# Optimization experiments

Measured on AMD Instinct MI355X. Metric: run time of the kernel, lower is better.

Reference implementation:

```python
import jax, jax.numpy as jnp
import numpy as np

B, N, D, H = 32, 64, 128, 256
LN_EPS = 1e-5


def _mlp(x, W1, b1, g, beta, W2, b2):
    # Linear -> LayerNorm -> GELU (exact erf) -> Linear
    h = x @ W1 + b1
    mu = jnp.mean(h, axis=-1, keepdims=True)
    var = jnp.var(h, axis=-1, keepdims=True)
    h = (h - mu) * jax.lax.rsqrt(var + LN_EPS) * g + beta
    h = jax.nn.gelu(h, approximate=False)
    return h @ W2 + b2


def setup_inputs() -> dict:
    key = jax.random.key(0)
    ks = jax.random.split(key, 10)
    s = lambda fan_in: 1.0 / np.sqrt(fan_in)
    return {
        "slots": jax.random.normal(ks[0], (B, N, D), dtype=jnp.float32),
        "adjacency": jax.random.uniform(ks[1], (B, N, N), dtype=jnp.float32),
        # edge_net params
        "We1": jax.random.uniform(ks[2], (2 * D, H), minval=-s(2 * D), maxval=s(2 * D), dtype=jnp.float32),
        "be1": jnp.zeros((H,), jnp.float32),
        "ge": jnp.ones((H,), jnp.float32),
        "bge": jnp.zeros((H,), jnp.float32),
        "We2": jax.random.uniform(ks[3], (H, D), minval=-s(H), maxval=s(H), dtype=jnp.float32),
        "be2": jnp.zeros((D,), jnp.float32),
        # node_net params
        "Wn1": jax.random.uniform(ks[4], (2 * D, H), minval=-s(2 * D), maxval=s(2 * D), dtype=jnp.float32),
        "bn1": jnp.zeros((H,), jnp.float32),
        "gn": jnp.ones((H,), jnp.float32),
        "bgn": jnp.zeros((H,), jnp.float32),
        "Wn2": jax.random.uniform(ks[5], (H, D), minval=-s(H), maxval=s(H), dtype=jnp.float32),
        "bn2": jnp.zeros((D,), jnp.float32),
    }


def reference(slots, adjacency, We1, be1, ge, bge, We2, be2, Wn1, bn1, gn, bgn, Wn2, bn2):
    b, n, d = slots.shape
    # all-pairs edge features: receiver i, sender j -> [B,N,N,2D]
    ei = jnp.broadcast_to(slots[:, :, None, :], (b, n, n, d))
    ej = jnp.broadcast_to(slots[:, None, :, :], (b, n, n, d))
    edge_feat = jnp.concatenate([ei, ej], axis=-1)
    edge_out = _mlp(edge_feat, We1, be1, ge, bge, We2, be2)  # [B,N,N,D]
    # mask diagonal (i != j) and weight by adjacency, then reduce over j
    mask = 1.0 - jnp.eye(n, dtype=slots.dtype)
    w = adjacency * mask  # [B,N,N]
    messages = jnp.einsum('bij,bijd->bid', w, edge_out)
    node_input = jnp.concatenate([slots, messages], axis=-1)
    delta = _mlp(node_input, Wn1, bn1, gn, bgn, Wn2, bn2)
    return slots + delta
```

## Files before the change

### kernel.cpp

```cpp
#include <hip/hip_runtime.h>

#define NB 32
#define NN 64
#define ND 128
#define NH 256
#define LN_EPS 1e-5f
#define RP 4

__device__ __forceinline__ float gelu2(float x) {
    const float au = fabsf(x);
    const float z  = au * 0.70710678118654752440f;
    float p = fmaf(0.078108f, z, 0.000972f);
    p = fmaf(p, z, 0.230389f);
    p = fmaf(p, z, 0.278393f);
    p = fmaf(p, z, 1.0f);
    const float p2 = p * p;
    const float r  = __builtin_amdgcn_rcpf(p2 * p2);
    return (x + au) - au * r;
}
__device__ __forceinline__ float gelu_h(float x) { return 0.5f * gelu2(x); }

__global__ __launch_bounds__(256) void k_pre(const float* __restrict__ slots,
                                             const float* __restrict__ We1,
                                             const float* __restrict__ be1,
                                             const float* __restrict__ Wn1,
                                             const float* __restrict__ We2,
                                             const float* __restrict__ be2,
                                             float* __restrict__ Pt,
                                             float* __restrict__ Qm,
                                             float* __restrict__ XW,
                                             float4* __restrict__ rowstats,
                                             float* __restrict__ WC,
                                             float* __restrict__ v) {
    __shared__ float xs[RP][ND];
    __shared__ float red[4][RP][4];
    const int t = threadIdx.x;

    if (blockIdx.x >= 512) {
        const int bid2 = blockIdx.x - 512;
        if (bid2 == 64) {
            __shared__ float bs[ND];
            if (t < ND) bs[t] = be2[t];
            __syncthreads();
            float acc = 0.f;
            #pragma unroll 4
            for (int d = 0; d < ND; ++d) acc = fmaf(bs[d], Wn1[(ND + d) * NH + t], acc);
            v[t] = acc;
            return;
        }
        const int k0 = bid2 * 4;
        __shared__ float ws[4][ND];
        #pragma unroll
        for (int i = 0; i < 2; ++i) {
            const int idx = t + i * 256;
            ws[idx >> 7][idx & 127] = We2[(k0 + (idx >> 7)) * ND + (idx & 127)];
        }
        __syncthreads();
        float acc[4] = {0.f, 0.f, 0.f, 0.f};
        #pragma unroll 4
        for (int d = 0; d < ND; ++d) {
            const float wn = Wn1[(ND + d) * NH + t];
            #pragma unroll
            for (int r = 0; r < 4; ++r) acc[r] = fmaf(ws[r][d], wn, acc[r]);
        }
        #pragma unroll
        for (int r = 0; r < 4; ++r) WC[(k0 + r) * NH + t] = acc[r];
        return;
    }

    const int r0 = blockIdx.x * RP;
    const int lane = t & 63, wave = t >> 6;
    #pragma unroll
    for (int i = 0; i < 2; ++i) {
        const int idx = t + i * 256;
        xs[idx >> 7][idx & 127] = slots[(size_t)(r0 + (idx >> 7)) * ND + (idx & 127)];
    }
    __syncthreads();
    float pt[RP], qq[RP], xw[RP];
    const float bb = be1[t];
    #pragma unroll
    for (int r = 0; r < RP; ++r) { pt[r] = bb; qq[r] = 0.f; xw[r] = 0.f; }
    #pragma unroll 4
    for (int d = 0; d < ND; ++d) {
        const float wt  = We1[d * NH + t];
        const float wbt = We1[(ND + d) * NH + t];
        const float wn  = Wn1[d * NH + t];
        #pragma unroll
        for (int r = 0; r < RP; ++r) {
            const float x = xs[r][d];
            pt[r] = fmaf(x, wt,  pt[r]);
            qq[r] = fmaf(x, wbt, qq[r]);
            xw[r] = fmaf(x, wn,  xw[r]);
        }
    }
    #pragma unroll
    for (int r = 0; r < RP; ++r) {
        const size_t row = (size_t)(r0 + r);
        Pt[row * NH + t] = pt[r];
        Qm[row * NH + t] = qq[r];
        XW[row * NH + t] = xw[r];
    }
    float s1[RP], s2[RP], s3[RP], s4[RP];
    #pragma unroll
    for (int r = 0; r < RP; ++r) {
        s1[r] = pt[r]; s2[r] = pt[r] * pt[r];
        s3[r] = qq[r]; s4[r] = qq[r] * qq[r];
    }
    #pragma unroll
    for (int off = 32; off; off >>= 1) {
        #pragma unroll
        for (int r = 0; r < RP; ++r) {
            s1[r] += __shfl_xor(s1[r], off);
            s2[r] += __shfl_xor(s2[r], off);
            s3[r] += __shfl_xor(s3[r], off);
            s4[r] += __shfl_xor(s4[r], off);
        }
    }
    if (lane == 0) {
        #pragma unroll
        for (int r = 0; r < RP; ++r) {
            red[wave][r][0] = s1[r]; red[wave][r][1] = s2[r];
            red[wave][r][2] = s3[r]; red[wave][r][3] = s4[r];
        }
    }
    __syncthreads();
    if (t < RP) {
        float4 st;
        st.x = (red[0][t][0] + red[1][t][0]) + (red[2][t][0] + red[3][t][0]);
        st.y = (red[0][t][1] + red[1][t][1]) + (red[2][t][1] + red[3][t][1]);
        st.z = (red[0][t][2] + red[1][t][2]) + (red[2][t][2] + red[3][t][2]);
        st.w = (red[0][t][3] + red[1][t][3]) + (red[2][t][3] + red[3][t][3]);
        rowstats[r0 + t] = st;
    }
}

__global__ __launch_bounds__(256) void k_msg(
    const float* __restrict__ adj,
    const float* __restrict__ Pt,
    const float* __restrict__ Qm,
    const float4* __restrict__ rowstats,
    const float* __restrict__ ge,  const float* __restrict__ bge,
    float* __restrict__ Sw, float* __restrict__ wsumw)
{
    __shared__ float  lds_pt[NH];
    __shared__ float4 lds_wmr[NN];
    __shared__ float  lds_s[4][NH];

    const int row = blockIdx.x;
    const int b   = row >> 6;
    const int i   = row & 63;
    const int t   = threadIdx.x;
    const int lane = t & 63;
    const int wave = t >> 6;

    lds_pt[t] = Pt[(size_t)row * NH + t];
    __syncthreads();

    const int jp = t >> 2, part = t & 3;
    {
        float cd = 0.f;
        const float4* qrow = (const float4*)(Qm + ((size_t)b * NN + jp) * NH) + part * 16;
        const float4* pr   = (const float4*)lds_pt + part * 16;
        #pragma unroll 4
        for (int k = 0; k < 16; ++k) {
            const float4 q = qrow[k];
            const float4 p = pr[k];
            cd = fmaf(p.x, q.x, fmaf(p.y, q.y, fmaf(p.z, q.z, fmaf(p.w, q.w, cd))));
        }
        cd += __shfl_xor(cd, 1); cd += __shfl_xor(cd, 2);
        if (part == 0) {
            const float inv = 1.0f / NH;
            const float4 stj = rowstats[(size_t)b * NN + jp];
            const float4 sti = rowstats[row];
            float a = adj[(size_t)row * NN + jp];
            if (jp == i) a = 0.f;
            const float mu = (sti.x + stj.z) * inv;
            const float e2 = fmaf(2.f, cd, sti.y + stj.w) * inv;
            const float rr = __builtin_amdgcn_rsqf(fmaf(-mu, mu, e2) + LN_EPS);
            lds_wmr[jp] = make_float4(0.5f * a, rr, -mu * rr, a);
        }
    }
    __syncthreads();

    if (wave == 0) {
        float wv = lds_wmr[lane].w;
        #pragma unroll
        for (int off = 32; off; off >>= 1) wv += __shfl_xor(wv, off);
        if (lane == 0) wsumw[row] = wv;
    }

    const float4 P  = ((const float4*)lds_pt)[lane];
    const float4 G  = ((const float4*)ge)[lane];
    const float4 Bg = ((const float4*)bge)[lane];
    const float4* Qb = (const float4*)(Qm + (size_t)b * NN * NH);
    float4 A = make_float4(0.f, 0.f, 0.f, 0.f);
    #pragma unroll 4
    for (int jj = wave; jj < NN; jj += 4) {
        const float4 q = Qb[jj * (NH / 4) + lane];
        const float4 m = lds_wmr[jj];
        float h, u0, u;
        h = P.x + q.x; u0 = fmaf(h, m.y, m.z); u = fmaf(u0, G.x, Bg.x); A.x = fmaf(m.x, gelu2(u), A.x);
        h = P.y + q.y; u0 = fmaf(h, m.y, m.z); u = fmaf(u0, G.y, Bg.y); A.y = fmaf(m.x, gelu2(u), A.y);
        h = P.z + q.z; u0 = fmaf(h, m.y, m.z); u = fmaf(u0, G.z, Bg.z); A.z = fmaf(m.x, gelu2(u), A.z);
        h = P.w + q.w; u0 = fmaf(h, m.y, m.z); u = fmaf(u0, G.w, Bg.w); A.w = fmaf(m.x, gelu2(u), A.w);
    }
    ((float4*)lds_s[wave])[lane] = A;
    __syncthreads();
    Sw[(size_t)row * NH + t] =
        (lds_s[0][t] + lds_s[1][t]) + (lds_s[2][t] + lds_s[3][t]);
}

__global__ __launch_bounds__(512) void k_node(
    const float* __restrict__ slots,
    const float* __restrict__ Sw, const float* __restrict__ wsumw,
    const float* __restrict__ XW,
    const float* __restrict__ WC, const float* __restrict__ v,
    const float* __restrict__ bn1,
    const float* __restrict__ gn,  const float* __restrict__ bgn,
    const float* __restrict__ Wn2, const float* __restrict__ bn2,
    float* __restrict__ out)
{
    __shared__ float lds_S[4][NH];
    __shared__ float lds_part[4][NH];
    __shared__ float lds_g[4][NH];
    __shared__ float lds_red[4][4][2];
    __shared__ float lds_mr[4][2];

    const int r0   = blockIdx.x * 4;
    const int t    = threadIdx.x;
    const int c    = t & 255;
    const int kh   = t >> 8;
    const int lane = t & 63;
    const int wave = t >> 6;

    lds_S[kh * 2 + 0][c] = Sw[(size_t)(r0 + kh * 2 + 0) * NH + c];
    lds_S[kh * 2 + 1][c] = Sw[(size_t)(r0 + kh * 2 + 1) * NH + c];
    __syncthreads();

    float acc[4] = {0.f, 0.f, 0.f, 0.f};
    {
        const float* wc = WC + (size_t)kh * 128 * NH + c;
        #pragma unroll 8
        for (int k = 0; k < 128; ++k) {
            const float w = wc[k * NH];
            const int kk = kh * 128 + k;
            acc[0] = fmaf(lds_S[0][kk], w, acc[0]);
            acc[1] = fmaf(lds_S[1][kk], w, acc[1]);
            acc[2] = fmaf(lds_S[2][kk], w, acc[2]);
            acc[3] = fmaf(lds_S[3][kk], w, acc[3]);
        }
    }
    if (kh == 1) {
        #pragma unroll
        for (int r = 0; r < 4; ++r) lds_part[r][c] = acc[r];
    }
    __syncthreads();

    float h[4];
    if (kh == 0) {
        const float b1 = bn1[c], vc = v[c];
        #pragma unroll
        for (int r = 0; r < 4; ++r)
            h[r] = acc[r] + lds_part[r][c] + fmaf(wsumw[r0 + r], vc, b1)
                 + XW[(size_t)(r0 + r) * NH + c];
        float s1[4], s2[4];
        #pragma unroll
        for (int r = 0; r < 4; ++r) { s1[r] = h[r]; s2[r] = h[r] * h[r]; }
        #pragma unroll
        for (int off = 32; off; off >>= 1) {
            #pragma unroll
            for (int r = 0; r < 4; ++r) {
                s1[r] += __shfl_xor(s1[r], off);
                s2[r] += __shfl_xor(s2[r], off);
            }
        }
        if (lane == 0) {
            #pragma unroll
            for (int r = 0; r < 4; ++r) { lds_red[wave][r][0] = s1[r]; lds_red[wave][r][1] = s2[r]; }
        }
    }
    __syncthreads();
    if (t < 4) {
        const float S1 = (lds_red[0][t][0] + lds_red[1][t][0]) + (lds_red[2][t][0] + lds_red[3][t][0]);
        const float S2 = (lds_red[0][t][1] + lds_red[1][t][1]) + (lds_red[2][t][1] + lds_red[3][t][1]);
        const float mu  = S1 * (1.0f / NH);
        const float var = fmaf(-mu, mu, S2 * (1.0f / NH));
        lds_mr[t][0] = mu;
        lds_mr[t][1] = __builtin_amdgcn_rsqf(var + LN_EPS);
    }
    __syncthreads();
    if (kh == 0) {
        const float g = gn[c], bg = bgn[c];
        #pragma unroll
        for (int r = 0; r < 4; ++r) {
            const float rr = lds_mr[r][1];
            const float u0 = fmaf(h[r], rr, -lds_mr[r][0] * rr);
            lds_g[r][c] = gelu_h(fmaf(u0, g, bg));
        }
    }
    __syncthreads();

    {
        const int rg = t >> 7, c2 = t & 127;
        float da = 0.f, db = 0.f;
        const float* w2 = Wn2 + c2;
        const float* gr = lds_g[rg];
        #pragma unroll 8
        for (int k = 0; k < NH; k += 2) {
            da = fmaf(gr[k],     w2[k * ND],       da);
            db = fmaf(gr[k + 1], w2[(k + 1) * ND], db);
        }
        const size_t o = (size_t)(r0 + rg) * ND + c2;
        out[o] = slots[o] + bn2[c2] + da + db;
    }
}

extern "C" void kernel_launch(void* const* d_in, const int* in_sizes, int n_in,
                              void* d_out, int out_size, void* d_ws, size_t ws_size,
                              hipStream_t stream) {
    const float* slots = (const float*)d_in[0];
    const float* adj   = (const float*)d_in[1];
    const float* We1   = (const float*)d_in[2];
    const float* be1   = (const float*)d_in[3];
    const float* ge    = (const float*)d_in[4];
    const float* bge   = (const float*)d_in[5];
    const float* We2   = (const float*)d_in[6];
    const float* be2   = (const float*)d_in[7];
    const float* Wn1   = (const float*)d_in[8];
    const float* bn1   = (const float*)d_in[9];
    const float* gn    = (const float*)d_in[10];
    const float* bgn   = (const float*)d_in[11];
    const float* Wn2   = (const float*)d_in[12];
    const float* bn2   = (const float*)d_in[13];
    float* out = (float*)d_out;

    const size_t RN = (size_t)NB * NN;
    float*  Ptw   = (float*)d_ws;
    float*  Qw    = Ptw   + RN * NH;
    float*  XWw   = Qw    + RN * NH;
    float*  Sww   = XWw   + RN * NH;
    float*  wsumw = Sww   + RN * NH;
    float*  WCw   = wsumw + RN;
    float*  vw    = WCw   + (size_t)NH * NH;
    float4* rsw   = (float4*)(vw + NH);

    k_pre <<<577,          256, 0, stream>>>(slots, We1, be1, Wn1, We2, be2,
                                             Ptw, Qw, XWw, rsw, WCw, vw);
    k_msg <<<(int)RN,      256, 0, stream>>>(adj, Ptw, Qw, rsw, ge, bge, Sww, wsumw);
    k_node<<<(int)(RN / 4), 512, 0, stream>>>(slots, Sww, wsumw, XWw, WCw, vw,
                                              bn1, gn, bgn, Wn2, bn2, out);
}
```

Measured before the change: 62.72 us.

## Estrin GELU polynomial, occupancy hint, unroll tweaks, split-K float4 Wn2 GEMV

The GELU erf polynomial is re-evaluated in Estrin form to shorten the dependency chain. k_msg gets a min-blocks-per-CU launch bound and a fixed-trip loop with a pre-offset pointer. Unroll factors grow in k_pre and k_node. The final Wn2 product in k_node is split four ways over K with float4 weight loads, then reduced through shared memory. This costs an extra barrier and LDS buffer and may raise register pressure.

New measurement: 68.09 us. +8.6%, slower.

```diff
diff --git a/kernel.cpp b/kernel.cpp
--- a/kernel.cpp
+++ b/kernel.cpp
@@ -8,15 +8,16 @@
 #define RP 4
 
 __device__ __forceinline__ float gelu2(float x) {
-    const float au = fabsf(x);
-    const float z  = au * 0.70710678118654752440f;
-    float p = fmaf(0.078108f, z, 0.000972f);
-    p = fmaf(p, z, 0.230389f);
-    p = fmaf(p, z, 0.278393f);
-    p = fmaf(p, z, 1.0f);
-    const float p2 = p * p;
-    const float r  = __builtin_amdgcn_rcpf(p2 * p2);
-    return (x + au) - au * r;
+    const float au  = fabsf(x);
+    const float xpa = x + au;
+    const float z   = au * 0.70710678118654752440f;
+    const float z2  = z * z;
+    const float pc  = fmaf(0.078108f, z, 0.000972f);
+    const float pb  = fmaf(0.278393f, z, 1.0f);
+    const float p   = fmaf(z2, fmaf(z, pc, 0.230389f), pb);
+    const float p2  = p * p;
+    const float r   = __builtin_amdgcn_rcpf(p2 * p2);
+    return fmaf(-au, r, xpa);
 }
 __device__ __forceinline__ float gelu_h(float x) { return 0.5f * gelu2(x); }
 
@@ -80,7 +81,7 @@
     const float bb = be1[t];
     #pragma unroll
     for (int r = 0; r < RP; ++r) { pt[r] = bb; qq[r] = 0.f; xw[r] = 0.f; }
-    #pragma unroll 4
+    #pragma unroll 8
     for (int d = 0; d < ND; ++d) {
         const float wt  = We1[d * NH + t];
         const float wbt = We1[(ND + d) * NH + t];
@@ -134,7 +135,7 @@
     }
 }
 
-__global__ __launch_bounds__(256) void k_msg(
+__global__ __launch_bounds__(256, 8) void k_msg(
     const float* __restrict__ adj,
     const float* __restrict__ Pt,
     const float* __restrict__ Qm,
@@ -192,17 +193,18 @@
     const float4 P  = ((const float4*)lds_pt)[lane];
     const float4 G  = ((const float4*)ge)[lane];
     const float4 Bg = ((const float4*)bge)[lane];
-    const float4* Qb = (const float4*)(Qm + (size_t)b * NN * NH);
+    const float4* Qb = (const float4*)(Qm + (size_t)b * NN * NH) + lane;
     float4 A = make_float4(0.f, 0.f, 0.f, 0.f);
     #pragma unroll 4
-    for (int jj = wave; jj < NN; jj += 4) {
-        const float4 q = Qb[jj * (NH / 4) + lane];
+    for (int k = 0; k < 16; ++k) {
+        const int jj = wave + 4 * k;
+        const float4 q = Qb[jj * (NH / 4)];
         const float4 m = lds_wmr[jj];
-        float h, u0, u;
-        h = P.x + q.x; u0 = fmaf(h, m.y, m.z); u = fmaf(u0, G.x, Bg.x); A.x = fmaf(m.x, gelu2(u), A.x);
-        h = P.y + q.y; u0 = fmaf(h, m.y, m.z); u = fmaf(u0, G.y, Bg.y); A.y = fmaf(m.x, gelu2(u), A.y);
-        h = P.z + q.z; u0 = fmaf(h, m.y, m.z); u = fmaf(u0, G.z, Bg.z); A.z = fmaf(m.x, gelu2(u), A.z);
-        h = P.w + q.w; u0 = fmaf(h, m.y, m.z); u = fmaf(u0, G.w, Bg.w); A.w = fmaf(m.x, gelu2(u), A.w);
+        float h, u;
+        h = P.x + q.x; u = fmaf(fmaf(h, m.y, m.z), G.x, Bg.x); A.x = fmaf(m.x, gelu2(u), A.x);
+        h = P.y + q.y; u = fmaf(fmaf(h, m.y, m.z), G.y, Bg.y); A.y = fmaf(m.x, gelu2(u), A.y);
+        h = P.z + q.z; u = fmaf(fmaf(h, m.y, m.z), G.z, Bg.z); A.z = fmaf(m.x, gelu2(u), A.z);
+        h = P.w + q.w; u = fmaf(fmaf(h, m.y, m.z), G.w, Bg.w); A.w = fmaf(m.x, gelu2(u), A.w);
     }
     ((float4*)lds_s[wave])[lane] = A;
     __syncthreads();
@@ -223,6 +225,7 @@
     __shared__ float lds_S[4][NH];
     __shared__ float lds_part[4][NH];
     __shared__ float lds_g[4][NH];
+    __shared__ float lds_d[4][4][ND];
     __shared__ float lds_red[4][4][2];
     __shared__ float lds_mr[4][2];
 
@@ -240,7 +243,7 @@
     float acc[4] = {0.f, 0.f, 0.f, 0.f};
     {
         const float* wc = WC + (size_t)kh * 128 * NH + c;
-        #pragma unroll 8
+        #pragma unroll 16
         for (int k = 0; k < 128; ++k) {
             const float w = wc[k * NH];
             const int kk = kh * 128 + k;
@@ -301,17 +304,31 @@
     __syncthreads();
 
     {
+        const int r  = t >> 7;
+        const int ks = (t >> 5) & 3;
+        const int cg = t & 31;
+        float4 dacc = make_float4(0.f, 0.f, 0.f, 0.f);
+        const float4* w2 = (const float4*)Wn2 + cg;
+        const float*  gr = lds_g[r];
+        const int kbeg = ks * 64;
+        #pragma unroll 8
+        for (int k = kbeg; k < kbeg + 64; ++k) {
+            const float4 w = w2[k * (ND / 4)];
+            const float gv = gr[k];
+            dacc.x = fmaf(gv, w.x, dacc.x);
+            dacc.y = fmaf(gv, w.y, dacc.y);
+            dacc.z = fmaf(gv, w.z, dacc.z);
+            dacc.w = fmaf(gv, w.w, dacc.w);
+        }
+        ((float4*)lds_d[r][ks])[cg] = dacc;
+    }
+    __syncthreads();
+    {
         const int rg = t >> 7, c2 = t & 127;
-        float da = 0.f, db = 0.f;
-        const float* w2 = Wn2 + c2;
-        const float* gr = lds_g[rg];
-        #pragma unroll 8
-        for (int k = 0; k < NH; k += 2) {
-            da = fmaf(gr[k],     w2[k * ND],       da);
-            db = fmaf(gr[k + 1], w2[(k + 1) * ND], db);
-        }
+        const float dsum = (lds_d[rg][0][c2] + lds_d[rg][1][c2])
+                         + (lds_d[rg][2][c2] + lds_d[rg][3][c2]);
         const size_t o = (size_t)(r0 + rg) * ND + c2;
-        out[o] = slots[o] + bn2[c2] + da + db;
+        out[o] = slots[o] + bn2[c2] + dsum;
     }
 }
 
@@ -344,9 +361,9 @@
     float*  vw    = WCw   + (size_t)NH * NH;
     float4* rsw   = (float4*)(vw + NH);
 
-    k_pre <<<577,          256, 0, stream>>>(slots, We1, be1, Wn1, We2, be2,
-                                             Ptw, Qw, XWw, rsw, WCw, vw);
-    k_msg <<<(int)RN,      256, 0, stream>>>(adj, Ptw, Qw, rsw, ge, bge, Sww, wsumw);
+    k_pre <<<577,           256, 0, stream>>>(slots, We1, be1, Wn1, We2, be2,
+                                              Ptw, Qw, XWw, rsw, WCw, vw);
+    k_msg <<<(int)RN,       256, 0, stream>>>(adj, Ptw, Qw, rsw, ge, bge, Sww, wsumw);
     k_node<<<(int)(RN / 4), 512, 0, stream>>>(slots, Sww, wsumw, XWw, WCw, vw,
                                               bn1, gn, bgn, Wn2, bn2, out);
 }
```
